# Kernel tuning notes

Hardware: AMD Instinct MI355X
Metric: run time of the kernel (lower is better)

Reference implementation:

```python
import jax, jax.numpy as jnp
import numpy as np

E = 64        # num_experts
T = 65536     # num_tokens (sum of group_sizes)
D_IN = 512    # in_features
D_OUT = 512   # out_features


def setup_inputs() -> dict:
    key = jax.random.key(0)
    k1, k2, k3 = jax.random.split(key, 3)
    inputs = jax.random.normal(k1, (T, D_IN), dtype=jnp.float32)
    # lecun_normal init scale for kernel
    kernel = jax.random.normal(k2, (E, D_IN, D_OUT), dtype=jnp.float32) * (1.0 / np.sqrt(D_IN))
    bias = jax.random.normal(k3, (D_OUT,), dtype=jnp.float32) * 0.02
    # equal-size contiguous per-expert token groups, summing to T
    group_sizes = jnp.full((E,), T // E, dtype=jnp.int32)
    return {"inputs": inputs, "kernel": kernel, "bias": bias, "group_sizes": group_sizes}


def reference(inputs, kernel, bias, group_sizes):
    # Grouped (ragged) matmul: tokens are laid out contiguously by expert;
    # group_sizes[e] tokens are multiplied by kernel[e]. This is exactly
    # jax.lax.ragged_dot (megablocks-style grouped GEMM semantics).
    y = jax.lax.ragged_dot(inputs, kernel, group_sizes)  # [T, D_OUT]
    return y + bias[None, :]
```

## Files before the change

### kernel.cpp

```cpp
#include <hip/hip_runtime.h>
#include <hip/hip_bf16.h>

#define NUM_E 64
#define D_K 512
#define D_N 512
#define BM 128
#define BN 128
#define MAX_TILES 576
#define GRID_X (MAX_TILES * 4)

typedef __bf16 bf16x8 __attribute__((ext_vector_type(8)));
typedef float f32x16 __attribute__((ext_vector_type(16)));
typedef float f32x4 __attribute__((ext_vector_type(4)));
typedef unsigned int u32;
typedef unsigned short u16;

__device__ __forceinline__ int imin(int a, int b) { return a < b ? a : b; }

__device__ __forceinline__ void gll16(const void* g, void* l) {
    __builtin_amdgcn_global_load_lds(
        (const __attribute__((address_space(1))) u32*)(uintptr_t)g,
        (__attribute__((address_space(3))) u32*)(uintptr_t)l, 16, 0, 0);
}

__device__ __forceinline__ void cvt_split(float a, u32 &hi, u32 &lo) {
    u32 u  = __float_as_uint(a);
    u32 rh = (u + 0x7FFFu + ((u >> 16) & 1u)) & 0xFFFF0000u;
    hi = rh >> 16;
    float res = a - __uint_as_float(rh);
    lo = __float_as_uint(res) >> 16;
}

__global__ void build_tiles_kernel(const int* __restrict__ gs,
                                   int* __restrict__ cnt,
                                   int* __restrict__ desc) {
    int e = threadIdx.x;
    if (e >= NUM_E) return;
    int row = 0, toff = 0;
    for (int i = 0; i < e; ++i) {
        int g = gs[i];
        row += g;
        toff += (g + BM - 1) / BM;
    }
    int g = gs[e];
    int nt = (g + BM - 1) / BM;
    for (int i = 0; i < nt; ++i) {
        int b = 3 * (toff + i);
        desc[b]     = e;
        desc[b + 1] = row + i * BM;
        desc[b + 2] = imin(BM, g - i * BM);
    }
    if (e == NUM_E - 1) cnt[0] = toff + nt;
}

__global__ void convert_x_kernel(const float* __restrict__ X, u16* __restrict__ Xc,
                                 int nocts) {
    int idx = blockIdx.x * blockDim.x + threadIdx.x;
    int stride = gridDim.x * blockDim.x;
    for (int o = idx; o < nocts; o += stride) {
        int row = o >> 6;
        int c8  = (o & 63) * 8;
        const float* p = X + (size_t)o * 8;
        f32x4 v0 = *(const f32x4*)p;
        f32x4 v1 = *(const f32x4*)(p + 4);
        u32 h[8], l[8];
        #pragma unroll
        for (int j = 0; j < 4; ++j) cvt_split(v0[j], h[j], l[j]);
        #pragma unroll
        for (int j = 0; j < 4; ++j) cvt_split(v1[j], h[4 + j], l[4 + j]);
        uint4 hp, lp;
        hp.x = h[0] | (h[1] << 16); hp.y = h[2] | (h[3] << 16);
        hp.z = h[4] | (h[5] << 16); hp.w = h[6] | (h[7] << 16);
        lp.x = l[0] | (l[1] << 16); lp.y = l[2] | (l[3] << 16);
        lp.z = l[4] | (l[5] << 16); lp.w = l[6] | (l[7] << 16);
        *(uint4*)(Xc + (size_t)row * 1024 + c8)       = hp;
        *(uint4*)(Xc + (size_t)row * 1024 + 512 + c8) = lp;
    }
}

__global__ void convert_w_kernel(const float* __restrict__ W, u16* __restrict__ Wc) {
    __shared__ float Tf[64 * 68];
    int bid = blockIdx.x;
    int e  = bid >> 6;
    int ti = (bid >> 3) & 7;
    int tj = bid & 7;
    int tid = threadIdx.x;

    const float* Wp = W + (size_t)e * D_K * D_N + (size_t)(ti * 64) * D_N + tj * 64;
    #pragma unroll
    for (int it = 0; it < 4; ++it) {
        int kl = it * 16 + (tid >> 4);
        int nl = (tid & 15) * 4;
        f32x4 v = *(const f32x4*)(Wp + (size_t)kl * D_N + nl);
        #pragma unroll
        for (int j = 0; j < 4; ++j) Tf[(nl + j) * 68 + kl] = v[j];
    }
    __syncthreads();
    #pragma unroll
    for (int it = 0; it < 2; ++it) {
        int nl = it * 32 + (tid >> 3);
        int ko = (tid & 7) * 8;
        f32x4 a = *(const f32x4*)(Tf + nl * 68 + ko);
        f32x4 b = *(const f32x4*)(Tf + nl * 68 + ko + 4);
        u32 h[8], l[8];
        #pragma unroll
        for (int j = 0; j < 4; ++j) cvt_split(a[j], h[j], l[j]);
        #pragma unroll
        for (int j = 0; j < 4; ++j) cvt_split(b[j], h[4 + j], l[4 + j]);
        uint4 hp, lp;
        hp.x = h[0] | (h[1] << 16); hp.y = h[2] | (h[3] << 16);
        hp.z = h[4] | (h[5] << 16); hp.w = h[6] | (h[7] << 16);
        lp.x = l[0] | (l[1] << 16); lp.y = l[2] | (l[3] << 16);
        lp.z = l[4] | (l[5] << 16); lp.w = l[6] | (l[7] << 16);
        u16* outp = Wc + ((size_t)e << 19) + (size_t)(tj * 64 + nl) * 1024 + ti * 64 + ko;
        *(uint4*)outp         = hp;
        *(uint4*)(outp + 512) = lp;
    }
}

__global__ void __launch_bounds__(256, 2)
gemm_split_kernel(const u16* __restrict__ Xc, const u16* __restrict__ Wc,
                  const float* __restrict__ bias, const int* __restrict__ cnt,
                  const int* __restrict__ desc, float* __restrict__ out, int T) {
    __shared__ u16 As[2][BM * 64];
    __shared__ u16 Bs[2][BN * 64];

    int bid = blockIdx.x;
    int s = (bid & 7) * (GRID_X / 8) + (bid >> 3);
    int tile  = s >> 2;
    int ntile = s & 3;
    if (tile >= cnt[0]) return;

    int expert = desc[3 * tile];
    int row0   = desc[3 * tile + 1];
    int rows   = desc[3 * tile + 2];
    int n0 = ntile * BN;

    const int tid  = threadIdx.x;
    const int lane = tid & 63;
    const int wid  = tid >> 6;
    const int wm = wid >> 1, wn = wid & 1;
    const int lr = lane & 31, kg = lane >> 5;

    int aoff[4], boff[4], ldsb[4];
    #pragma unroll
    for (int c = 0; c < 4; ++c) {
        int chunk = c * 256 + tid;
        int r = chunk >> 3, j = chunk & 7;
        int cb = (j * 16) ^ ((r & 7) << 4);
        int ar = imin(row0 + r, T - 1);
        aoff[c] = ar * 1024 + (cb >> 1);
        boff[c] = (expert << 19) + (n0 + r) * 1024 + (cb >> 1);
        ldsb[c] = (c * 256 + wid * 64) * 16;
    }

    f32x16 acc[2][2];
    #pragma unroll
    for (int i = 0; i < 2; ++i)
        #pragma unroll
        for (int j = 0; j < 2; ++j)
            #pragma unroll
            for (int r = 0; r < 16; ++r) acc[i][j][r] = 0.0f;

    #pragma unroll
    for (int c = 0; c < 4; ++c) {
        gll16(Xc + aoff[c], (char*)As[0] + ldsb[c]);
        gll16(Wc + boff[c], (char*)Bs[0] + ldsb[c]);
    }

    for (int t = 0; t < 24; ++t) {
        int cur = t & 1;
        if (t < 23) {
            int tn  = t + 1;
            int tt  = tn & 7, seg = tn >> 3;
            int acol = tt * 64 + (seg == 2 ? 512 : 0);
            int bcol = tt * 64 + (seg == 1 ? 512 : 0);
            int nxt = cur ^ 1;
            #pragma unroll
            for (int c = 0; c < 4; ++c) {
                gll16(Xc + aoff[c] + acol, (char*)As[nxt] + ldsb[c]);
                gll16(Wc + boff[c] + bcol, (char*)Bs[nxt] + ldsb[c]);
            }
            asm volatile("s_waitcnt vmcnt(8)" ::: "memory");
        } else {
            asm volatile("s_waitcnt vmcnt(0)" ::: "memory");
        }
        __builtin_amdgcn_s_barrier();

        const char* Ab = (const char*)As[cur];
        const char* Bb = (const char*)Bs[cur];
        #pragma unroll
        for (int ks = 0; ks < 4; ++ks) {
            int kb = ks * 32 + kg * 16;
            bf16x8 af[2], bb[2];
            #pragma unroll
            for (int f = 0; f < 2; ++f) {
                int ra = wm * 64 + f * 32 + lr;
                af[f] = *(const bf16x8*)(Ab + ra * 128 + (kb ^ ((ra & 7) << 4)));
                int rb = wn * 64 + f * 32 + lr;
                bb[f] = *(const bf16x8*)(Bb + rb * 128 + (kb ^ ((rb & 7) << 4)));
            }
            #pragma unroll
            for (int i = 0; i < 2; ++i)
                #pragma unroll
                for (int j = 0; j < 2; ++j)
                    acc[i][j] = __builtin_amdgcn_mfma_f32_32x32x16_bf16(af[i], bb[j], acc[i][j], 0, 0, 0);
        }
        asm volatile("" ::: "memory");
        __builtin_amdgcn_s_barrier();
    }

    #pragma unroll
    for (int j = 0; j < 2; ++j) {
        int col = n0 + wn * 64 + j * 32 + lr;
        float bv = bias[col];
        #pragma unroll
        for (int i = 0; i < 2; ++i) {
            #pragma unroll
            for (int r = 0; r < 16; ++r) {
                int lm = wm * 64 + i * 32 + (r & 3) + 8 * (r >> 2) + 4 * kg;
                if (lm < rows)
                    out[(size_t)(row0 + lm) * D_N + col] = acc[i][j][r] + bv;
            }
        }
    }
}

#define KPAD 72
__global__ void __launch_bounds__(256, 2)
grouped_gemm_fallback(const float* __restrict__ X, const float* __restrict__ W,
                      const float* __restrict__ bias, const int* __restrict__ cnt,
                      const int* __restrict__ desc, float* __restrict__ out) {
    extern __shared__ u16 lds[];
    u16* Ahi = lds;
    u16* Alo = Ahi + BM * KPAD;
    u16* Bhi = Alo + BM * KPAD;
    u16* Blo = Bhi + BM * KPAD;

    int bid = blockIdx.x;
    int s = (bid & 7) * (GRID_X / 8) + (bid >> 3);
    int tile  = s >> 2;
    int ntile = s & 3;
    if (tile >= cnt[0]) return;

    int expert = desc[3 * tile];
    int row0   = desc[3 * tile + 1];
    int rows   = desc[3 * tile + 2];
    int n0 = ntile * BN;

    const int tid  = threadIdx.x;
    const int lane = tid & 63;
    const int wid  = tid >> 6;
    const int wm = wid >> 1, wn = wid & 1;
    const int lr = lane & 31, kg = lane >> 5;

    const float* Wp = W + (size_t)expert * D_K * D_N;

    f32x16 acc[2][2];
    #pragma unroll
    for (int i = 0; i < 2; ++i)
        #pragma unroll
        for (int j = 0; j < 2; ++j)
            #pragma unroll
            for (int r = 0; r < 16; ++r) acc[i][j][r] = 0.0f;

    for (int kt = 0; kt < D_K / 64; ++kt) {
        int k0 = kt * 64;
        #pragma unroll
        for (int it = 0; it < 8; ++it) {
            int idx = it * 256 + tid;
            int m = idx >> 4, q = idx & 15;
            f32x4 v;
            if (m < rows) v = *(const f32x4*)(X + (size_t)(row0 + m) * D_K + k0 + q * 4);
            else          v[0] = v[1] = v[2] = v[3] = 0.0f;
            u32 h[4], l[4];
            #pragma unroll
            for (int j = 0; j < 4; ++j) cvt_split(v[j], h[j], l[j]);
            uint2 hp, lp;
            hp.x = h[0] | (h[1] << 16); hp.y = h[2] | (h[3] << 16);
            lp.x = l[0] | (l[1] << 16); lp.y = l[2] | (l[3] << 16);
            *(uint2*)(Ahi + m * KPAD + q * 4) = hp;
            *(uint2*)(Alo + m * KPAD + q * 4) = lp;
        }
        #pragma unroll
        for (int it = 0; it < 8; ++it) {
            int idx = it * 256 + tid;
            int n = idx & 127, kb = idx >> 7;
            const float* bp = Wp + (size_t)(k0 + kb * 4) * D_N + n0 + n;
            u32 h[4], l[4];
            #pragma unroll
            for (int j = 0; j < 4; ++j) { float b = bp[(size_t)j * D_N]; cvt_split(b, h[j], l[j]); }
            uint2 hp, lp;
            hp.x = h[0] | (h[1] << 16); hp.y = h[2] | (h[3] << 16);
            lp.x = l[0] | (l[1] << 16); lp.y = l[2] | (l[3] << 16);
            *(uint2*)(Bhi + n * KPAD + kb * 4) = hp;
            *(uint2*)(Blo + n * KPAD + kb * 4) = lp;
        }
        __syncthreads();
        #pragma unroll
        for (int ks = 0; ks < 4; ++ks) {
            bf16x8 ah[2], al[2], bh[2], bl[2];
            #pragma unroll
            for (int f = 0; f < 2; ++f) {
                int aoff2 = (wm * 64 + f * 32 + lr) * KPAD + ks * 16 + kg * 8;
                ah[f] = *(const bf16x8*)(Ahi + aoff2);
                al[f] = *(const bf16x8*)(Alo + aoff2);
                int boff2 = (wn * 64 + f * 32 + lr) * KPAD + ks * 16 + kg * 8;
                bh[f] = *(const bf16x8*)(Bhi + boff2);
                bl[f] = *(const bf16x8*)(Blo + boff2);
            }
            #pragma unroll
            for (int i = 0; i < 2; ++i)
                #pragma unroll
                for (int j = 0; j < 2; ++j) {
                    acc[i][j] = __builtin_amdgcn_mfma_f32_32x32x16_bf16(ah[i], bh[j], acc[i][j], 0, 0, 0);
                    acc[i][j] = __builtin_amdgcn_mfma_f32_32x32x16_bf16(ah[i], bl[j], acc[i][j], 0, 0, 0);
                    acc[i][j] = __builtin_amdgcn_mfma_f32_32x32x16_bf16(al[i], bh[j], acc[i][j], 0, 0, 0);
                }
        }
        __syncthreads();
    }
    #pragma unroll
    for (int j = 0; j < 2; ++j) {
        int col = n0 + wn * 64 + j * 32 + lr;
        float bv = bias[col];
        #pragma unroll
        for (int i = 0; i < 2; ++i) {
            #pragma unroll
            for (int r = 0; r < 16; ++r) {
                int lm = wm * 64 + i * 32 + (r & 3) + 8 * (r >> 2) + 4 * kg;
                if (lm < rows)
                    out[(size_t)(row0 + lm) * D_N + col] = acc[i][j][r] + bv;
            }
        }
    }
}

extern "C" void kernel_launch(void* const* d_in, const int* in_sizes, int n_in,
                              void* d_out, int out_size, void* d_ws, size_t ws_size,
                              hipStream_t stream) {
    const float* X    = (const float*)d_in[0];
    const float* W    = (const float*)d_in[1];
    const float* bias = (const float*)d_in[2];
    const int*   gs   = (const int*)d_in[3];
    float* out = (float*)d_out;

    int T = in_sizes[0] / D_K;

    int* cnt  = (int*)d_ws;
    int* desc = cnt + 4;
    hipLaunchKernelGGL(build_tiles_kernel, dim3(1), dim3(64), 0, stream, gs, cnt, desc);

    size_t x_bytes = (size_t)T * 1024 * sizeof(u16);
    size_t w_bytes = (size_t)NUM_E * D_N * 1024 * sizeof(u16);
    size_t need = 8192 + x_bytes + w_bytes;

    if (ws_size >= need) {
        u16* Xc = (u16*)((char*)d_ws + 8192);
        u16* Wc = (u16*)((char*)d_ws + 8192 + x_bytes);

        int nocts = T * (D_K / 8);
        hipLaunchKernelGGL(convert_x_kernel, dim3(2048), dim3(256), 0, stream, X, Xc, nocts);
        hipLaunchKernelGGL(convert_w_kernel, dim3(NUM_E * 64), dim3(256), 0, stream, W, Wc);
        hipLaunchKernelGGL(gemm_split_kernel, dim3(GRID_X), dim3(256), 0, stream,
                           Xc, Wc, bias, cnt, desc, out, T);
    } else {
        const size_t lds_bytes = (size_t)4 * BM * KPAD * sizeof(u16);
        hipLaunchKernelGGL(grouped_gemm_fallback, dim3(GRID_X), dim3(256), lds_bytes, stream,
                           X, W, bias, cnt, desc, out);
    }
}
```

Measured before the change: 463.4 us.

## Load hi and lo split tiles together and drop LDS double buffering

The GEMM loop is restructured so each k-chunk loads the high and low bf16 halves of both A and B into one wider LDS tile. All three split-precision MFMAs (hi*hi, hi*lo, lo*hi) then run from a single load, in 8 iterations instead of 24 passes over the data. The goal is to reuse each loaded hi fragment across two products and cut the number of barrier-separated steps. In exchange, the double-buffered prefetch is removed, so global loads no longer overlap with MFMA work. The swizzle also changes to 16 rows.

```diff
diff --git a/kernel.cpp b/kernel.cpp
--- a/kernel.cpp
+++ b/kernel.cpp
@@ -122,8 +122,8 @@
 gemm_split_kernel(const u16* __restrict__ Xc, const u16* __restrict__ Wc,
                   const float* __restrict__ bias, const int* __restrict__ cnt,
                   const int* __restrict__ desc, float* __restrict__ out, int T) {
-    __shared__ u16 As[2][BM * 64];
-    __shared__ u16 Bs[2][BN * 64];
+    __shared__ u16 As[BM * 128];
+    __shared__ u16 Bs[BN * 128];
 
     int bid = blockIdx.x;
     int s = (bid & 7) * (GRID_X / 8) + (bid >> 3);
@@ -142,15 +142,16 @@
     const int wm = wid >> 1, wn = wid & 1;
     const int lr = lane & 31, kg = lane >> 5;
 
-    int aoff[4], boff[4], ldsb[4];
-    #pragma unroll
-    for (int c = 0; c < 4; ++c) {
+    int aoff[8], boff[8], ldsb[8];
+    #pragma unroll
+    for (int c = 0; c < 8; ++c) {
         int chunk = c * 256 + tid;
-        int r = chunk >> 3, j = chunk & 7;
-        int cb = (j * 16) ^ ((r & 7) << 4);
+        int r = chunk >> 4, j = chunk & 15;
+        int cb = (j * 16) ^ ((r & 15) << 4);
+        int inrow = (cb < 128) ? (cb >> 1) : (512 + ((cb - 128) >> 1));
         int ar = imin(row0 + r, T - 1);
-        aoff[c] = ar * 1024 + (cb >> 1);
-        boff[c] = (expert << 19) + (n0 + r) * 1024 + (cb >> 1);
+        aoff[c] = ar * 1024 + inrow;
+        boff[c] = (expert << 19) + (n0 + r) * 1024 + inrow;
         ldsb[c] = (c * 256 + wid * 64) * 16;
     }
 
@@ -162,52 +163,40 @@
             #pragma unroll
             for (int r = 0; r < 16; ++r) acc[i][j][r] = 0.0f;
 
-    #pragma unroll
-    for (int c = 0; c < 4; ++c) {
-        gll16(Xc + aoff[c], (char*)As[0] + ldsb[c]);
-        gll16(Wc + boff[c], (char*)Bs[0] + ldsb[c]);
-    }
-
-    for (int t = 0; t < 24; ++t) {
-        int cur = t & 1;
-        if (t < 23) {
-            int tn  = t + 1;
-            int tt  = tn & 7, seg = tn >> 3;
-            int acol = tt * 64 + (seg == 2 ? 512 : 0);
-            int bcol = tt * 64 + (seg == 1 ? 512 : 0);
-            int nxt = cur ^ 1;
-            #pragma unroll
-            for (int c = 0; c < 4; ++c) {
-                gll16(Xc + aoff[c] + acol, (char*)As[nxt] + ldsb[c]);
-                gll16(Wc + boff[c] + bcol, (char*)Bs[nxt] + ldsb[c]);
-            }
-            asm volatile("s_waitcnt vmcnt(8)" ::: "memory");
-        } else {
-            asm volatile("s_waitcnt vmcnt(0)" ::: "memory");
-        }
-        __builtin_amdgcn_s_barrier();
-
-        const char* Ab = (const char*)As[cur];
-        const char* Bb = (const char*)Bs[cur];
+    for (int kc = 0; kc < 8; ++kc) {
+        int ksrc = kc * 64;
+        #pragma unroll
+        for (int c = 0; c < 8; ++c) {
+            gll16(Xc + aoff[c] + ksrc, (char*)As + ldsb[c]);
+            gll16(Wc + boff[c] + ksrc, (char*)Bs + ldsb[c]);
+        }
+        __syncthreads();
+
         #pragma unroll
         for (int ks = 0; ks < 4; ++ks) {
             int kb = ks * 32 + kg * 16;
-            bf16x8 af[2], bb[2];
+            bf16x8 ah[2], al[2], bh[2], bl[2];
             #pragma unroll
             for (int f = 0; f < 2; ++f) {
                 int ra = wm * 64 + f * 32 + lr;
-                af[f] = *(const bf16x8*)(Ab + ra * 128 + (kb ^ ((ra & 7) << 4)));
+                int swa = (ra & 15) << 4;
+                ah[f] = *(const bf16x8*)((const char*)As + ra * 256 + (kb ^ swa));
+                al[f] = *(const bf16x8*)((const char*)As + ra * 256 + ((128 | kb) ^ swa));
                 int rb = wn * 64 + f * 32 + lr;
-                bb[f] = *(const bf16x8*)(Bb + rb * 128 + (kb ^ ((rb & 7) << 4)));
+                int swb = (rb & 15) << 4;
+                bh[f] = *(const bf16x8*)((const char*)Bs + rb * 256 + (kb ^ swb));
+                bl[f] = *(const bf16x8*)((const char*)Bs + rb * 256 + ((128 | kb) ^ swb));
             }
             #pragma unroll
             for (int i = 0; i < 2; ++i)
                 #pragma unroll
-                for (int j = 0; j < 2; ++j)
-                    acc[i][j] = __builtin_amdgcn_mfma_f32_32x32x16_bf16(af[i], bb[j], acc[i][j], 0, 0, 0);
-        }
-        asm volatile("" ::: "memory");
-        __builtin_amdgcn_s_barrier();
+                for (int j = 0; j < 2; ++j) {
+                    acc[i][j] = __builtin_amdgcn_mfma_f32_32x32x16_bf16(ah[i], bh[j], acc[i][j], 0, 0, 0);
+                    acc[i][j] = __builtin_amdgcn_mfma_f32_32x32x16_bf16(ah[i], bl[j], acc[i][j], 0, 0, 0);
+                    acc[i][j] = __builtin_amdgcn_mfma_f32_32x32x16_bf16(al[i], bh[j], acc[i][j], 0, 0, 0);
+                }
+        }
+        __syncthreads();
     }
 
     #pragma unroll
```

Result: no change. 458.1 us (-1.1%).
